# Performance work log

Measured on AMD Instinct MI355X. Metric: run time of the kernel, lower is better.

The kernel has to match this reference:

```python
import jax, jax.numpy as jnp
import numpy as np


def _conv1x1(x, w, b):
    # x:[B,C,H,W], w:[O,C,1,1], b:[O]
    y = jax.lax.conv_general_dilated(x, w, (1, 1), 'SAME',
                                     dimension_numbers=('NCHW', 'OIHW', 'NCHW'))
    return y + b[None, :, None, None]


def _dwconv3x3(x, w, b):
    # depthwise: x:[B,C,H,W2], w:[C,1,3,3], b:[C]
    c = x.shape[1]
    y = jax.lax.conv_general_dilated(x, w, (1, 1), 'SAME',
                                     dimension_numbers=('NCHW', 'OIHW', 'NCHW'),
                                     feature_group_count=c)
    return y + b[None, :, None, None]


def setup_inputs() -> dict:
    key = jax.random.key(0)
    k1, k2, k3, k4, k5 = jax.random.split(key, 5)
    B, C, H, W = 4, 64, 256, 256
    x = jax.random.normal(k1, (B, C, H, W), dtype=jnp.float32)
    # qkv 1x1 conv params: [3C, C, 1, 1]
    w_qkv = jax.random.normal(k2, (3 * C, C, 1, 1), dtype=jnp.float32) * (1.0 / np.sqrt(C))
    b_qkv = jax.random.normal(k3, (3 * C,), dtype=jnp.float32) * 0.01
    # depthwise 3x3 conv params: [C, 1, 3, 3]
    w_dw = jax.random.normal(k4, (C, 1, 3, 3), dtype=jnp.float32) * (1.0 / 3.0)
    b_dw = jax.random.normal(k5, (C,), dtype=jnp.float32) * 0.01
    return {"x": x, "w_qkv": w_qkv, "b_qkv": b_qkv, "w_dw": w_dw, "b_dw": b_dw}


def reference(x, w_qkv, b_qkv, w_dw, b_dw):
    # qkv projection and split into q, k, v  (each [B,C,H,W])
    qkv = _conv1x1(x, w_qkv, b_qkv)
    q, k, v = jnp.split(qkv, 3, axis=1)
    # per-channel spatial attention scores: q @ k^T over last dim -> [B,C,H,H]
    scores = jnp.einsum('bchw,bcgw->bchg', q, k)
    # depthwise 3x3 conv on the [H,H] score map, then softmax over last dim
    attn = jax.nn.softmax(_dwconv3x3(scores, w_dw, b_dw), axis=-1)
    # attn @ v + residual -> [B,C,H,W]
    return jnp.einsum('bchg,bcgw->bchw', attn, v) + x
```

## Files before the change

### kernel.cpp

```cpp
#include <hip/hip_runtime.h>
#include <math.h>

#define B 4
#define C 64
#define H 256
#define W 256
#define HW (H*W)
#define CHW (C*HW)
#define BCHW (B*CHW)

typedef _Float16 half8v __attribute__((ext_vector_type(8)));
typedef float f32x4 __attribute__((ext_vector_type(4)));


__device__ inline ushort f16_bits(float f) {
    _Float16 h = (_Float16)f;
    return *(ushort*)&h;
}

#define LDS_BARRIER() do { \
    asm volatile("s_waitcnt lgkmcnt(0)" ::: "memory"); \
    __builtin_amdgcn_s_barrier(); \
} while (0)

__global__ __launch_bounds__(256, 4) void qkv_kernel(
    const float* __restrict__ x, const float* __restrict__ w,
    const float* __restrict__ bias, ushort* __restrict__ qkv)
{
    __shared__ ushort tile[2][32 * 264];
    int t = threadIdx.x;
    int lane = t & 63, wv = t >> 6;
    int l15 = lane & 15, l4 = lane >> 4;
    int p0 = blockIdx.x * 256;
    int b = p0 >> 16;
    int ppx = p0 & (HW - 1);
    int pxw = ppx + wv * 64;

    const float* xb = x + (size_t)b * CHW;

    half8v bfr[4][2];
    #pragma unroll
    for (int pf = 0; pf < 4; ++pf)
        #pragma unroll
        for (int kc = 0; kc < 2; ++kc) {
            int k0 = kc * 32 + l4 * 8;
            int px = pxw + pf * 16 + l15;
            half8v hv;
            #pragma unroll
            for (int j = 0; j < 8; ++j)
                hv[j] = (_Float16)xb[(size_t)(k0 + j) * HW + px];
            bfr[pf][kc] = hv;
        }

    auto load_afr = [&](int ocb, half8v afr[2][2]) {
        #pragma unroll
        for (int nf = 0; nf < 2; ++nf)
            #pragma unroll
            for (int kc = 0; kc < 2; ++kc) {
                int oc = ocb + nf * 16 + l15;
                int k0 = kc * 32 + l4 * 8;
                const float4* wp = (const float4*)&w[oc * 64 + k0];
                float4 wa = wp[0], wb2 = wp[1];
                half8v a;
                a[0] = (_Float16)wa.x;  a[1] = (_Float16)wa.y;
                a[2] = (_Float16)wa.z;  a[3] = (_Float16)wa.w;
                a[4] = (_Float16)wb2.x; a[5] = (_Float16)wb2.y;
                a[6] = (_Float16)wb2.z; a[7] = (_Float16)wb2.w;
                afr[nf][kc] = a;
            }
    };

    half8v afrA[2][2], afrB[2][2];
    load_afr(0, afrA);

    #pragma unroll
    for (int ch = 0; ch < 6; ++ch) {
        int ocb = ch * 32;
        half8v (*cur)[2] = (ch & 1) ? afrB : afrA;
        half8v (*nxt)[2] = (ch & 1) ? afrA : afrB;

        f32x4 acc[2][4];
        #pragma unroll
        for (int nf = 0; nf < 2; ++nf)
            #pragma unroll
            for (int pf = 0; pf < 4; ++pf) acc[nf][pf] = (f32x4)0.f;

        #pragma unroll
        for (int kc = 0; kc < 2; ++kc)
            #pragma unroll
            for (int nf = 0; nf < 2; ++nf)
                #pragma unroll
                for (int pf = 0; pf < 4; ++pf)
                    acc[nf][pf] = __builtin_amdgcn_mfma_f32_16x16x32_f16(
                        cur[nf][kc], bfr[pf][kc], acc[nf][pf], 0, 0, 0);

        if (ch < 5) load_afr(ocb + 32, nxt);

        ushort* tl = tile[ch & 1];
        #pragma unroll
        for (int nf = 0; nf < 2; ++nf)
            #pragma unroll
            for (int r = 0; r < 4; ++r) {
                int ocl = nf * 16 + l4 * 4 + r;
                float bv = bias[ocb + ocl];
                #pragma unroll
                for (int pf = 0; pf < 4; ++pf)
                    tl[ocl * 264 + wv * 64 + pf * 16 + l15] =
                        f16_bits(acc[nf][pf][r] + bv);
            }

        LDS_BARRIER();

        #pragma unroll
        for (int j = 0; j < 4; ++j) {
            int id = t + 256 * j;
            int row = id >> 5, seg = id & 31;
            uint4 val = *(const uint4*)&tl[row * 264 + seg * 8];
            int oc = ocb + row;
            ushort* dst = qkv + (size_t)(oc >> 6) * BCHW
                        + ((size_t)b * 64 + (oc & 63)) * HW + ppx + seg * 8;
            *(uint4*)dst = val;
        }
    }
}

#define SST 266
#define YST 268
#define ATS 264
#define SOT 264
#define VSTR 268

__global__ __launch_bounds__(512, 2) void fused_kernel(
    const ushort* __restrict__ qf, const ushort* __restrict__ kf,
    const ushort* __restrict__ vf,
    const float* __restrict__ wdw, const float* __restrict__ bdw,
    const float* __restrict__ x, float* __restrict__ out)
{
    __shared__ float sbuf[34 * SST];
    __shared__ ushort qlds[48 * 256];
    __shared__ float mxf[32];

    int t = threadIdx.x;
    int lane = t & 63, wv = t >> 6;
    int l15 = lane & 15, l4 = lane >> 4;
    int col = t & 255, half = t >> 8;
    int base = half * 16;

    int bc = blockIdx.x;
    int c = bc & 63;

    const ushort* qb = qf + (size_t)bc * HW;
    const ushort* kb = kf + (size_t)bc * HW;
    const ushort* vb = vf + (size_t)bc * HW;
    const float*  xb = x  + (size_t)bc * HW;
    float*        ob = out + (size_t)bc * HW;

    int g0 = wv * 32;

    half8v ka[2][8];
    {
        const ushort* kr0 = kb + (g0 + l15) * 256 + l4 * 8;
        const ushort* kr1 = kb + (g0 + 16 + l15) * 256 + l4 * 8;
        #pragma unroll
        for (int kc = 0; kc < 8; ++kc) {
            ka[0][kc] = *(const half8v*)(kr0 + kc * 32);
            ka[1][kc] = *(const half8v*)(kr1 + kc * 32);
        }
    }

    half8v va[2][8];
    {
        ushort* vstage = (ushort*)sbuf;
        #pragma unroll
        for (int hc = 0; hc < 4; ++hc) {
            #pragma unroll
            for (int s = 0; s < 4; ++s) {
                int id = t + s * 512;
                int row = id >> 5, seg = id & 31;
                *(uint4*)&vstage[row * VSTR + seg * 8] =
                    *(const uint4*)(vb + (hc * 64 + row) * 256 + seg * 8);
            }
            __syncthreads();
            #pragma unroll
            for (int gf = 0; gf < 2; ++gf)
                #pragma unroll
                for (int kcl = 0; kcl < 2; ++kcl) {
                    half8v v;
                    #pragma unroll
                    for (int j = 0; j < 8; ++j)
                        v[j] = *(const _Float16*)&vstage[(kcl * 32 + l4 * 8 + j) * VSTR
                                                         + g0 + gf * 16 + l15];
                    va[gf][hc * 2 + kcl] = v;
                }
            __syncthreads();
        }
    }

    float w00 = wdw[c*9+0], w01 = wdw[c*9+1], w02 = wdw[c*9+2];
    float w10 = wdw[c*9+3], w11 = wdw[c*9+4], w12 = wdw[c*9+5];
    float w20 = wdw[c*9+6], w21 = wdw[c*9+7], w22 = wdw[c*9+8];
    float bias = bdw[c];

    half8v ones;
    #pragma unroll
    for (int j = 0; j < 8; ++j) ones[j] = (_Float16)1.0f;

    #pragma unroll 1
    for (int tile = 0; tile < 8; ++tile) {
        int h0 = tile * 32;

        #pragma unroll
        for (int s = 0; s < 3; ++s) {
            int id = t + s * 512;
            int row = id >> 5, cch = id & 31;
            int hq = min(max(h0 - 1 + row, 0), 255);
            uint4 val = *(const uint4*)(qb + hq * 256 + cch * 8);
            *(uint4*)((char*)qlds + row * 512 + ((cch ^ (row & 7)) << 4)) = val;
        }
        LDS_BARRIER();

        {
            f32x4 acc[3][2];
            #pragma unroll
            for (int i = 0; i < 3; ++i)
                #pragma unroll
                for (int j = 0; j < 2; ++j) acc[i][j] = (f32x4)0.f;

            #pragma unroll
            for (int kc = 0; kc < 8; ++kc) {
                int ch4 = kc * 4 + l4;
                half8v q0 = *(const half8v*)((char*)qlds + (l15)      * 512 + ((ch4 ^ ( l15       & 7)) << 4));
                half8v q1 = *(const half8v*)((char*)qlds + (16 + l15) * 512 + ((ch4 ^ ((16 + l15) & 7)) << 4));
                half8v q2 = *(const half8v*)((char*)qlds + (32 + l15) * 512 + ((ch4 ^ ((32 + l15) & 7)) << 4));
                __builtin_amdgcn_s_setprio(1);
                acc[0][0] = __builtin_amdgcn_mfma_f32_16x16x32_f16(q0, ka[0][kc], acc[0][0], 0, 0, 0);
                acc[0][1] = __builtin_amdgcn_mfma_f32_16x16x32_f16(q0, ka[1][kc], acc[0][1], 0, 0, 0);
                acc[1][0] = __builtin_amdgcn_mfma_f32_16x16x32_f16(q1, ka[0][kc], acc[1][0], 0, 0, 0);
                acc[1][1] = __builtin_amdgcn_mfma_f32_16x16x32_f16(q1, ka[1][kc], acc[1][1], 0, 0, 0);
                acc[2][0] = __builtin_amdgcn_mfma_f32_16x16x32_f16(q2, ka[0][kc], acc[2][0], 0, 0, 0);
                acc[2][1] = __builtin_amdgcn_mfma_f32_16x16x32_f16(q2, ka[1][kc], acc[2][1], 0, 0, 0);
                __builtin_amdgcn_s_setprio(0);
            }
            #pragma unroll
            for (int hf = 0; hf < 3; ++hf)
                #pragma unroll
                for (int gf = 0; gf < 2; ++gf)
                    #pragma unroll
                    for (int r = 0; r < 4; ++r) {
                        int cr = hf * 16 + l4 * 4 + r;
                        if (cr < 34)
                            sbuf[cr * SST + g0 + gf * 16 + l15] = acc[hf][gf][r];
                    }
        }
        LDS_BARRIER();

        float y[16];
        {
            float l0, m0, r0, l1, m1, r1;
            if (base == 0 && h0 == 0) { l0 = m0 = r0 = 0.f; }
            else {
                m0 = sbuf[base * SST + col];
                l0 = (col > 0)   ? sbuf[base * SST + col - 1] : 0.f;
                r0 = (col < 255) ? sbuf[base * SST + col + 1] : 0.f;
            }
            m1 = sbuf[(base + 1) * SST + col];
            l1 = (col > 0)   ? sbuf[(base + 1) * SST + col - 1] : 0.f;
            r1 = (col < 255) ? sbuf[(base + 1) * SST + col + 1] : 0.f;

            #pragma unroll
            for (int i = 0; i < 16; ++i) {
                float l2, m2, r2;
                if (h0 + base + i + 1 < 256) {
                    int sl = (base + i + 2) * SST;
                    m2 = sbuf[sl + col];
                    l2 = (col > 0)   ? sbuf[sl + col - 1] : 0.f;
                    r2 = (col < 255) ? sbuf[sl + col + 1] : 0.f;
                } else { l2 = m2 = r2 = 0.f; }
                y[i] = bias
                     + w00*l0 + w01*m0 + w02*r0
                     + w10*l1 + w11*m1 + w12*r1
                     + w20*l2 + w21*m2 + w22*r2;
                l0 = l1; m0 = m1; r0 = r1;
                l1 = l2; m1 = m2; r1 = r2;
            }
        }
        LDS_BARRIER();

        float* yL = sbuf;
        #pragma unroll
        for (int i = 0; i < 16; ++i)
            yL[(base + i) * YST + col] = y[i];
        LDS_BARRIER();

        {
            int r = t >> 4, c16 = t & 15;
            const f32x4* p = (const f32x4*)&yL[r * YST + c16 * 16];
            f32x4 v0 = p[0], v1 = p[1], v2 = p[2], v3 = p[3];
            float m = v0[0];
            #pragma unroll
            for (int j = 1; j < 4; ++j) m = fmaxf(m, v0[j]);
            #pragma unroll
            for (int j = 0; j < 4; ++j) m = fmaxf(m, v1[j]);
            #pragma unroll
            for (int j = 0; j < 4; ++j) m = fmaxf(m, v2[j]);
            #pragma unroll
            for (int j = 0; j < 4; ++j) m = fmaxf(m, v3[j]);
            m = fmaxf(m, __shfl_xor(m, 1));
            m = fmaxf(m, __shfl_xor(m, 2));
            m = fmaxf(m, __shfl_xor(m, 4));
            m = fmaxf(m, __shfl_xor(m, 8));
            if (c16 == 0) mxf[r] = m;
        }
        LDS_BARRIER();

        ushort* attnb = (ushort*)sbuf;
        #pragma unroll
        for (int i = 0; i < 16; ++i) {
            float e = __expf(y[i] - mxf[base + i]);
            attnb[(base + i) * ATS + col] = f16_bits(e);
        }
        LDS_BARRIER();

        f32x4 pacc[2][2], accs[2];
        #pragma unroll
        for (int i = 0; i < 2; ++i) {
            accs[i] = (f32x4)0.f;
            #pragma unroll
            for (int j = 0; j < 2; ++j) pacc[i][j] = (f32x4)0.f;
        }

        #pragma unroll
        for (int kc = 0; kc < 8; ++kc) {
            half8v af0 = *(const half8v*)&attnb[l15 * ATS + kc * 32 + l4 * 8];
            half8v af1 = *(const half8v*)&attnb[(16 + l15) * ATS + kc * 32 + l4 * 8];
            __builtin_amdgcn_s_setprio(1);
            pacc[0][0] = __builtin_amdgcn_mfma_f32_16x16x32_f16(af0, va[0][kc], pacc[0][0], 0, 0, 0);
            pacc[0][1] = __builtin_amdgcn_mfma_f32_16x16x32_f16(af0, va[1][kc], pacc[0][1], 0, 0, 0);
            accs[0]    = __builtin_amdgcn_mfma_f32_16x16x32_f16(af0, ones, accs[0], 0, 0, 0);
            pacc[1][0] = __builtin_amdgcn_mfma_f32_16x16x32_f16(af1, va[0][kc], pacc[1][0], 0, 0, 0);
            pacc[1][1] = __builtin_amdgcn_mfma_f32_16x16x32_f16(af1, va[1][kc], pacc[1][1], 0, 0, 0);
            accs[1]    = __builtin_amdgcn_mfma_f32_16x16x32_f16(af1, ones, accs[1], 0, 0, 0);
            __builtin_amdgcn_s_setprio(0);
        }
        LDS_BARRIER();

        float* og = sbuf;
        #pragma unroll
        for (int hf = 0; hf < 2; ++hf)
            #pragma unroll
            for (int r = 0; r < 4; ++r) {
                int row = hf * 16 + l4 * 4 + r;
                float inv = 1.0f / accs[hf][r];
                #pragma unroll
                for (int wf = 0; wf < 2; ++wf)
                    og[row * SOT + g0 + wf * 16 + l15] = pacc[hf][wf][r] * inv;
            }
        LDS_BARRIER();

        #pragma unroll
        for (int s = 0; s < 4; ++s) {
            int id = t + s * 512;
            int row = id >> 6, seg = id & 63;
            f32x4 v = *(const f32x4*)&og[row * SOT + seg * 4];
            f32x4 xr = *(const f32x4*)&xb[(h0 + row) * 256 + seg * 4];
            v += xr;
            *(f32x4*)&ob[(h0 + row) * 256 + seg * 4] = v;
        }
    }
}

extern "C" void kernel_launch(void* const* d_in, const int* in_sizes, int n_in,
                              void* d_out, int out_size, void* d_ws, size_t ws_size,
                              hipStream_t stream)
{
    const float* x     = (const float*)d_in[0];
    const float* w_qkv = (const float*)d_in[1];
    const float* b_qkv = (const float*)d_in[2];
    const float* w_dw  = (const float*)d_in[3];
    const float* b_dw  = (const float*)d_in[4];

    ushort* qf = (ushort*)d_ws;
    ushort* kf = qf + (size_t)BCHW;
    ushort* vf = kf + (size_t)BCHW;
    float*  out = (float*)d_out;

    qkv_kernel  <<<B * HW / 256, 256, 0, stream>>>(x, w_qkv, b_qkv, qf);
    fused_kernel<<<B * C,        512, 0, stream>>>(qf, kf, vf, w_dw, b_dw, x, out);
}
```

Baseline: 113.4 us.

## Remap depthwise conv so each wavefront owns full rows, reducing max in-register

```diff
diff --git a/kernel.cpp b/kernel.cpp
--- a/kernel.cpp
+++ b/kernel.cpp
@@ -124,8 +124,7 @@
     }
 }
 
-#define SST 266
-#define YST 268
+#define SST 268
 #define ATS 264
 #define SOT 264
 #define VSTR 268
@@ -138,13 +137,12 @@
 {
     __shared__ float sbuf[34 * SST];
     __shared__ ushort qlds[48 * 256];
-    __shared__ float mxf[32];
 
     int t = threadIdx.x;
     int lane = t & 63, wv = t >> 6;
     int l15 = lane & 15, l4 = lane >> 4;
-    int col = t & 255, half = t >> 8;
-    int base = half * 16;
+    int col4 = t & 63, rg = t >> 6;
+    int c0 = col4 * 4;
 
     int bc = blockIdx.x;
     int c = bc & 63;
@@ -254,70 +252,68 @@
         }
         LDS_BARRIER();
 
-        float y[16];
+        float y[4][4], rmax[4];
         {
-            float l0, m0, r0, l1, m1, r1;
-            if (base == 0 && h0 == 0) { l0 = m0 = r0 = 0.f; }
-            else {
-                m0 = sbuf[base * SST + col];
-                l0 = (col > 0)   ? sbuf[base * SST + col - 1] : 0.f;
-                r0 = (col < 255) ? sbuf[base * SST + col + 1] : 0.f;
-            }
-            m1 = sbuf[(base + 1) * SST + col];
-            l1 = (col > 0)   ? sbuf[(base + 1) * SST + col - 1] : 0.f;
-            r1 = (col < 255) ? sbuf[(base + 1) * SST + col + 1] : 0.f;
-
-            #pragma unroll
-            for (int i = 0; i < 16; ++i) {
-                float l2, m2, r2;
-                if (h0 + base + i + 1 < 256) {
-                    int sl = (base + i + 2) * SST;
-                    m2 = sbuf[sl + col];
-                    l2 = (col > 0)   ? sbuf[sl + col - 1] : 0.f;
-                    r2 = (col < 255) ? sbuf[sl + col + 1] : 0.f;
-                } else { l2 = m2 = r2 = 0.f; }
-                y[i] = bias
-                     + w00*l0 + w01*m0 + w02*r0
-                     + w10*l1 + w11*m1 + w12*r1
-                     + w20*l2 + w21*m2 + w22*r2;
-                l0 = l1; m0 = m1; r0 = r1;
-                l1 = l2; m1 = m2; r1 = r2;
-            }
-        }
-        LDS_BARRIER();
-
-        float* yL = sbuf;
-        #pragma unroll
-        for (int i = 0; i < 16; ++i)
-            yL[(base + i) * YST + col] = y[i];
-        LDS_BARRIER();
-
-        {
-            int r = t >> 4, c16 = t & 15;
-            const f32x4* p = (const f32x4*)&yL[r * YST + c16 * 16];
-            f32x4 v0 = p[0], v1 = p[1], v2 = p[2], v3 = p[3];
-            float m = v0[0];
-            #pragma unroll
-            for (int j = 1; j < 4; ++j) m = fmaxf(m, v0[j]);
-            #pragma unroll
-            for (int j = 0; j < 4; ++j) m = fmaxf(m, v1[j]);
-            #pragma unroll
-            for (int j = 0; j < 4; ++j) m = fmaxf(m, v2[j]);
-            #pragma unroll
-            for (int j = 0; j < 4; ++j) m = fmaxf(m, v3[j]);
-            m = fmaxf(m, __shfl_xor(m, 1));
-            m = fmaxf(m, __shfl_xor(m, 2));
-            m = fmaxf(m, __shfl_xor(m, 4));
-            m = fmaxf(m, __shfl_xor(m, 8));
-            if (c16 == 0) mxf[r] = m;
+            f32x4 m0v, m1v, m2v;
+            float l0v, r0v, l1v, r1v, l2v, r2v;
+
+            auto rdrow = [&](int k, f32x4 &mv, float &lv, float &rv) {
+                int sr = rg * 4 + k;
+                bool valid = !((h0 == 0 && sr == 0) || (h0 + sr > 256));
+                f32x4 z = (f32x4)0.f;
+                mv = valid ? *(const f32x4*)&sbuf[sr * SST + c0] : z;
+                float le = __shfl_up(mv[3], 1);
+                float re = __shfl_down(mv[0], 1);
+                lv = (col4 == 0) ? 0.f : le;
+                rv = (col4 == 63) ? 0.f : re;
+            };
+
+            rdrow(0, m0v, l0v, r0v);
+            rdrow(1, m1v, l1v, r1v);
+            #pragma unroll
+            for (int k = 2; k < 6; ++k) {
+                rdrow(k, m2v, l2v, r2v);
+                int i = k - 2;
+                #pragma unroll
+                for (int j = 0; j < 4; ++j) {
+                    float a0 = (j == 0) ? l0v : m0v[j-1];
+                    float b0 = m0v[j];
+                    float e0 = (j == 3) ? r0v : m0v[j+1];
+                    float a1 = (j == 0) ? l1v : m1v[j-1];
+                    float b1 = m1v[j];
+                    float e1 = (j == 3) ? r1v : m1v[j+1];
+                    float a2 = (j == 0) ? l2v : m2v[j-1];
+                    float b2 = m2v[j];
+                    float e2 = (j == 3) ? r2v : m2v[j+1];
+                    y[i][j] = bias
+                        + w00*a0 + w01*b0 + w02*e0
+                        + w10*a1 + w11*b1 + w12*e1
+                        + w20*a2 + w21*b2 + w22*e2;
+                }
+                m0v = m1v; l0v = l1v; r0v = r1v;
+                m1v = m2v; l1v = l2v; r1v = r2v;
+            }
+
+            #pragma unroll
+            for (int i = 0; i < 4; ++i) {
+                float m = fmaxf(fmaxf(y[i][0], y[i][1]), fmaxf(y[i][2], y[i][3]));
+                #pragma unroll
+                for (int off = 32; off > 0; off >>= 1)
+                    m = fmaxf(m, __shfl_xor(m, off));
+                rmax[i] = m;
+            }
         }
         LDS_BARRIER();
 
         ushort* attnb = (ushort*)sbuf;
         #pragma unroll
-        for (int i = 0; i < 16; ++i) {
-            float e = __expf(y[i] - mxf[base + i]);
-            attnb[(base + i) * ATS + col] = f16_bits(e);
+        for (int i = 0; i < 4; ++i) {
+            int R = rg * 4 + i;
+            union { ushort u[4]; uint2 v; } pk;
+            #pragma unroll
+            for (int j = 0; j < 4; ++j)
+                pk.u[j] = f16_bits(__expf(y[i][j] - rmax[i]));
+            *(uint2*)&attnb[R * ATS + c0] = pk.v;
         }
         LDS_BARRIER();
 
```

New measurement: 109.6 us. -3.4%, faster.
